# Optimization experiments

Measured on AMD Instinct MI355X. Metric: run time of the kernel, lower is better.

The kernel has to match this reference:

```python
import jax, jax.numpy as jnp
import numpy as np

EPS = 1e-5

def _ln(x):
    m = jnp.mean(x, axis=-1, keepdims=True)
    v = jnp.mean((x - m) ** 2, axis=-1, keepdims=True)
    return (x - m) / jnp.sqrt(v + EPS)

def setup_inputs() -> dict:
    key = jax.random.key(0)
    ks = jax.random.split(key, 6)
    B, S, E, H = 2, 2048, 1024, 16
    sd = 1.0 / np.sqrt(E)
    x = jax.random.normal(ks[0], (B, S, E), dtype=jnp.float32)
    w_in = jax.random.normal(ks[1], (3 * E, E), dtype=jnp.float32) * sd
    w_out = jax.random.normal(ks[2], (E, E), dtype=jnp.float32) * sd
    w_fc = jax.random.normal(ks[3], (4 * E, E), dtype=jnp.float32) * sd
    b_fc = jnp.zeros((4 * E,), dtype=jnp.float32)
    w_proj = jax.random.normal(ks[4], (E, 4 * E), dtype=jnp.float32) * (1.0 / np.sqrt(4 * E))
    b_proj = jnp.zeros((E,), dtype=jnp.float32)
    return {"x": x, "w_in": w_in, "w_out": w_out, "w_fc": w_fc,
            "b_fc": b_fc, "w_proj": w_proj, "b_proj": b_proj}

def reference(x, w_in, w_out, w_fc, b_fc, w_proj, b_proj):
    B, S, E = x.shape
    H = 16
    D = E // H
    h = _ln(x)
    qkv = h @ w_in.T                      # [B,S,3E]
    q, k, v = jnp.split(qkv, 3, axis=-1)
    q = q.reshape(B, S, H, D)
    k = k.reshape(B, S, H, D)
    v = v.reshape(B, S, H, D)
    scale = 1.0 / np.sqrt(D)
    scores = jnp.einsum('bqhd,bkhd->bhqk', q, k) * scale  # [B,H,S,S]
    causal = jnp.tril(jnp.ones((S, S), dtype=bool))
    scores = jnp.where(causal, scores, -jnp.inf)
    attn = jax.nn.softmax(scores, axis=-1)
    o = jnp.einsum('bhqk,bkhd->bqhd', attn, v).reshape(B, S, E)
    attn_out = o @ w_out.T
    x2 = x + attn_out                      # residual 1
    h2 = _ln(x2)
    m = jax.nn.relu(h2 @ w_fc.T + b_fc)    # [B,S,4E]
    return (m @ w_proj.T + b_proj) + x2    # residual 2
```

## Files before the change

### kernel.cpp

```cpp
#include <hip/hip_runtime.h>
#include <stdint.h>

#define AS1 __attribute__((address_space(1)))
#define AS3 __attribute__((address_space(3)))

typedef __bf16 bf8_t __attribute__((ext_vector_type(8)));
typedef float f4_t __attribute__((ext_vector_type(4)));
typedef unsigned short ush;

__device__ __forceinline__ ush f2b(float f) {
  unsigned u = __builtin_bit_cast(unsigned, f);
  u += 0x7fffu + ((u >> 16) & 1u);
  return (ush)(u >> 16);
}
__device__ __forceinline__ void unpack8(uint4 u, float* dst) {
  unsigned a0 = u.x, a1 = u.y, a2 = u.z, a3 = u.w;
  dst[0] = __builtin_bit_cast(float, a0 << 16);
  dst[1] = __builtin_bit_cast(float, a0 & 0xffff0000u);
  dst[2] = __builtin_bit_cast(float, a1 << 16);
  dst[3] = __builtin_bit_cast(float, a1 & 0xffff0000u);
  dst[4] = __builtin_bit_cast(float, a2 << 16);
  dst[5] = __builtin_bit_cast(float, a2 & 0xffff0000u);
  dst[6] = __builtin_bit_cast(float, a3 << 16);
  dst[7] = __builtin_bit_cast(float, a3 & 0xffff0000u);
}

__global__ __launch_bounds__(256) void f2b_all(
    const float* __restrict__ w_in, const float* __restrict__ w_out,
    const float* __restrict__ w_fc, const float* __restrict__ w_proj,
    ush* __restrict__ o_in, ush* __restrict__ o_out,
    ush* __restrict__ o_fc, ush* __restrict__ o_proj) {
  const int blk = blockIdx.x;
  const float* src;
  ush* dst;
  int base;
  if (blk < 3072) { src = w_in; dst = o_in; base = blk; }
  else if (blk < 4096) { src = w_out; dst = o_out; base = blk - 3072; }
  else if (blk < 8192) { src = w_fc; dst = o_fc; base = blk - 4096; }
  else { src = w_proj; dst = o_proj; base = blk - 8192; }
  const int i = (base * 256 + threadIdx.x) * 4;
  float4 v = *(const float4*)(src + i);
  union { ush u[4]; uint2 d; } p;
  p.u[0] = f2b(v.x); p.u[1] = f2b(v.y); p.u[2] = f2b(v.z); p.u[3] = f2b(v.w);
  *(uint2*)(dst + i) = p.d;
}

__global__ __launch_bounds__(256) void ln_kernel(const float* __restrict__ x,
                                                 ush* __restrict__ out) {
  const int row = blockIdx.x, tid = threadIdx.x;
  const float* xr = x + (size_t)row * 1024;
  float4 v = ((const float4*)xr)[tid];
  float s = v.x + v.y + v.z + v.w;
  float q = v.x * v.x + v.y * v.y + v.z * v.z + v.w * v.w;
  for (int o = 32; o; o >>= 1) { s += __shfl_down(s, o); q += __shfl_down(q, o); }
  __shared__ float rs[4], rq[4];
  const int w = tid >> 6;
  if ((tid & 63) == 0) { rs[w] = s; rq[w] = q; }
  __syncthreads();
  s = rs[0] + rs[1] + rs[2] + rs[3];
  q = rq[0] + rq[1] + rq[2] + rq[3];
  const float mean = s * (1.0f / 1024.0f);
  const float var = q * (1.0f / 1024.0f) - mean * mean;
  const float rstd = rsqrtf(var + 1e-5f);
  union { ush u[4]; uint2 d; } p;
  p.u[0] = f2b((v.x - mean) * rstd);
  p.u[1] = f2b((v.y - mean) * rstd);
  p.u[2] = f2b((v.z - mean) * rstd);
  p.u[3] = f2b((v.w - mean) * rstd);
  *(uint2*)(out + (size_t)row * 1024 + tid * 4) = p.d;
}

template <int EPI, int BM, int MINW>
__global__ __launch_bounds__(256, MINW) void gemm_bt(
    const ush* __restrict__ A, const ush* __restrict__ Bw,
    int M, int N, int K,
    const float* __restrict__ bias, const float* __restrict__ resid,
    float* __restrict__ outF, ush* __restrict__ outB) {
  constexpr int MI = BM / 32;
  constexpr int NCH = (BM + 128) / 16;
  constexpr int PC = NCH / 4;
  constexpr int ASZ = BM * 32;
  __shared__ ush lds[2 * ASZ + 2 * 4096];
  const int tid = threadIdx.x;
  const int wave = tid >> 6, lane = tid & 63;
  const int bm = blockIdx.x, bn = blockIdx.y;
  const int wm = (wave & 1) * (BM / 2), wn = (wave >> 1) * 64;
  const int l16 = lane & 15, quad = lane >> 4;
  const int srow = lane >> 2;
  const int scol = (lane & 3) * 8;

  const ush* Abase = A + (size_t)(bm * BM) * K;
  const ush* Bbase = Bw + (size_t)(bn * 128) * K;

  f4_t acc[MI][4];
#pragma unroll
  for (int i = 0; i < MI; ++i)
#pragma unroll
    for (int j = 0; j < 4; ++j) acc[i][j] = (f4_t){0.f, 0.f, 0.f, 0.f};

  const int kiters = K >> 5;

  auto stage = [&](int k0, int buf) {
    const int kk = k0 * 32;
#pragma unroll
    for (int i = 0; i < PC; ++i) {
      const int c = wave * PC + i;
      if (c < BM / 16) {
        const ush* ga = Abase + (size_t)(c * 16 + srow) * K + kk + scol;
        __builtin_amdgcn_global_load_lds((const AS1 void*)ga,
                                         (AS3 void*)(lds + buf * ASZ + c * 512), 16, 0, 0);
      } else {
        const int c2 = c - BM / 16;
        const ush* gb = Bbase + (size_t)(c2 * 16 + srow) * K + kk + scol;
        __builtin_amdgcn_global_load_lds(
            (const AS1 void*)gb, (AS3 void*)(lds + 2 * ASZ + buf * 4096 + c2 * 512), 16, 0, 0);
      }
    }
  };

  stage(0, 0);
  __syncthreads();
  for (int k0 = 0; k0 < kiters; ++k0) {
    const int cur = k0 & 1;
    if (k0 + 1 < kiters) stage(k0 + 1, cur ^ 1);
    bf8_t af[MI], bfr[4];
#pragma unroll
    for (int mi = 0; mi < MI; ++mi)
      af[mi] = *(const bf8_t*)&lds[cur * ASZ + (wm + mi * 16 + l16) * 32 + quad * 8];
#pragma unroll
    for (int ni = 0; ni < 4; ++ni)
      bfr[ni] = *(const bf8_t*)&lds[2 * ASZ + cur * 4096 + (wn + ni * 16 + l16) * 32 + quad * 8];
#pragma unroll
    for (int mi = 0; mi < MI; ++mi)
#pragma unroll
      for (int ni = 0; ni < 4; ++ni)
        acc[mi][ni] =
            __builtin_amdgcn_mfma_f32_16x16x32_bf16(af[mi], bfr[ni], acc[mi][ni], 0, 0, 0);
    __syncthreads();
  }

  if (EPI == 0 || EPI == 2) {
    ush* eb = lds + wave * ASZ;
#pragma unroll
    for (int mi = 0; mi < MI; ++mi)
#pragma unroll
      for (int ni = 0; ni < 4; ++ni) {
        const int gn = bn * 128 + wn + ni * 16 + l16;
        const float bv = (EPI == 2) ? bias[gn] : 0.0f;
#pragma unroll
        for (int r = 0; r < 4; ++r) {
          float v = acc[mi][ni][r] + bv;
          if (EPI == 2) v = fmaxf(v, 0.0f);
          eb[(mi * 16 + quad * 4 + r) * 64 + ni * 16 + l16] = f2b(v);
        }
      }
#pragma unroll
    for (int j = 0; j < BM / 16; ++j) {
      const int lr = j * 8 + (lane >> 3);
      const int c8 = (lane & 7) * 8;
      uint4 v = *(const uint4*)&eb[lr * 64 + c8];
      *(uint4*)(outB + (size_t)(bm * BM + wm + lr) * N + bn * 128 + wn + c8) = v;
    }
  } else {
#pragma unroll
    for (int mi = 0; mi < MI; ++mi) {
#pragma unroll
      for (int ni = 0; ni < 4; ++ni) {
        const int gm0 = bm * BM + wm + mi * 16 + quad * 4;
        const int gn = bn * 128 + wn + ni * 16 + l16;
        const float bv = (EPI == 3) ? bias[gn] : 0.0f;
#pragma unroll
        for (int r = 0; r < 4; ++r) {
          const size_t idx = (size_t)(gm0 + r) * N + gn;
          outF[idx] = acc[mi][ni][r] + bv + resid[idx];
        }
      }
    }
  }
}

__global__ __launch_bounds__(256) void pack_kv(const ush* __restrict__ qkv,
                                               ush* __restrict__ Kp,
                                               ush* __restrict__ Vp) {
  const int lin = blockIdx.x;
  const int kt = lin & 31, h = (lin >> 5) & 15, b = lin >> 9;
  const int tid = threadIdx.x;
  __shared__ ush Vs[64 * 72];
  const size_t rowbase = (size_t)(b * 2048 + kt * 64) * 3072 + h * 64;
  ush* Kt = Kp + (size_t)lin * 4096;
  ush* Vt = Vp + (size_t)lin * 4096;

  const int r0 = tid >> 3, cin = tid & 7;
#pragma unroll
  for (int it = 0; it < 2; ++it) {
    const int r = r0 + it * 32;
    uint4 ku = *(const uint4*)(qkv + rowbase + (size_t)r * 3072 + 1024 + cin * 8);
    float f[8]; unpack8(ku, f);
    union { ush us[8]; uint4 v; } pk;
#pragma unroll
    for (int j = 0; j < 8; ++j) pk.us[j] = f2b(f[j] * 0.125f);
    *(uint4*)(Kt + (size_t)(r * 8 + (cin ^ (r & 7))) * 8) = pk.v;
    uint4 vu = *(const uint4*)(qkv + rowbase + (size_t)r * 3072 + 2048 + cin * 8);
    *(uint4*)&Vs[r * 72 + cin * 8] = vu;
  }
  __syncthreads();
#pragma unroll
  for (int oc2 = 0; oc2 < 2; ++oc2) {
    const int oc = tid * 2 + oc2;
    const int d = oc >> 3, c = oc & 7;
    const int k0 = 8 * (c ^ (d & 7));
    union { ush us[8]; uint4 v; } pk;
#pragma unroll
    for (int j = 0; j < 8; ++j) pk.us[j] = Vs[(k0 + j) * 72 + d];
    *(uint4*)(Vt + (size_t)oc * 8) = pk.v;
  }
}

__global__ __launch_bounds__(256, 4) void attn_kernel(const ush* __restrict__ qkv,
                                                      const ush* __restrict__ Kp,
                                                      const ush* __restrict__ Vp,
                                                      ush* __restrict__ o) {
  const int lin = blockIdx.x;
  const int b = lin & 1, h = (lin >> 1) & 15, tq = lin >> 5;
  const int tid = threadIdx.x;
  const int wave = tid >> 6, lane = tid & 63;
  const int l15 = lane & 15, quad = lane >> 4;

  __shared__ __align__(16) ush Ks[64 * 64];
  __shared__ __align__(16) ush Vt[64 * 64];
  __shared__ __align__(16) ush Ps[64 * 72];

  bf8_t qf[2];
  {
    const int qrow = b * 2048 + tq * 64 + wave * 16 + l15;
#pragma unroll
    for (int s = 0; s < 2; ++s) {
      union { uint4 u; bf8_t v; } pk;
      pk.u = *(const uint4*)(qkv + (size_t)qrow * 3072 + h * 64 + s * 32 + quad * 8);
      qf[s] = pk.v;
    }
  }

  float m_s = -1e30f, l_s = 0.f;
  f4_t O[4];
#pragma unroll
  for (int j = 0; j < 4; ++j) O[j] = (f4_t){0.f, 0.f, 0.f, 0.f};

  const int qw0 = tq * 64 + wave * 16;
  const int swz = (l15 & 7) * 8;
  const size_t tile0 = (size_t)((b * 16 + h) * 32) * 4096;

  for (int kt = 0; kt <= tq; ++kt) {
    __syncthreads();
    const ush* Ktile = Kp + tile0 + (size_t)kt * 4096;
    const ush* Vtile = Vp + tile0 + (size_t)kt * 4096;
#pragma unroll
    for (int i = 0; i < 2; ++i) {
      const int seg = wave * 2 + i;
      __builtin_amdgcn_global_load_lds((const AS1 void*)(Ktile + seg * 512 + lane * 8),
                                       (AS3 void*)(Ks + seg * 512), 16, 0, 0);
      __builtin_amdgcn_global_load_lds((const AS1 void*)(Vtile + seg * 512 + lane * 8),
                                       (AS3 void*)(Vt + seg * 512), 16, 0, 0);
    }
    __syncthreads();

    f4_t S[4];
#pragma unroll
    for (int mi = 0; mi < 4; ++mi) S[mi] = (f4_t){0.f, 0.f, 0.f, 0.f};
#pragma unroll
    for (int s = 0; s < 2; ++s)
#pragma unroll
      for (int mi = 0; mi < 4; ++mi) {
        bf8_t kf = *(const bf8_t*)&Ks[(mi * 16 + l15) * 64 + (((4 * s + quad) * 8) ^ swz)];
        S[mi] = __builtin_amdgcn_mfma_f32_16x16x32_bf16(kf, qf[s], S[mi], 0, 0, 0);
      }

    if (kt == tq) {
#pragma unroll
      for (int mi = 0; mi < 4; ++mi)
#pragma unroll
        for (int r = 0; r < 4; ++r) {
          const int kg = kt * 64 + mi * 16 + quad * 4 + r;
          const int qg = qw0 + l15;
          if (kg > qg) S[mi][r] = -1e30f;
        }
    }

    float mx = -1e30f;
#pragma unroll
    for (int mi = 0; mi < 4; ++mi)
#pragma unroll
      for (int r = 0; r < 4; ++r) mx = fmaxf(mx, S[mi][r]);
    mx = fmaxf(mx, __shfl_xor(mx, 16));
    mx = fmaxf(mx, __shfl_xor(mx, 32));
    const float mn = fmaxf(m_s, mx);
    const float alpha = __expf(m_s - mn);
    float sum = 0.f;
#pragma unroll
    for (int mi = 0; mi < 4; ++mi)
#pragma unroll
      for (int r = 0; r < 4; ++r) {
        const float p = __expf(S[mi][r] - mn);
        S[mi][r] = p;
        sum += p;
      }
    sum += __shfl_xor(sum, 16);
    sum += __shfl_xor(sum, 32);
    m_s = mn;
    l_s = l_s * alpha + sum;
#pragma unroll
    for (int mi = 0; mi < 4; ++mi) {
      uint2 w2;
      w2.x = (unsigned)f2b(S[mi][0]) | ((unsigned)f2b(S[mi][1]) << 16);
      w2.y = (unsigned)f2b(S[mi][2]) | ((unsigned)f2b(S[mi][3]) << 16);
      *(uint2*)&Ps[(wave * 16 + l15) * 72 + mi * 16 + quad * 4] = w2;
    }

    bf8_t pf[2], vf[4][2];
#pragma unroll
    for (int s = 0; s < 2; ++s)
      pf[s] = *(const bf8_t*)&Ps[(wave * 16 + l15) * 72 + s * 32 + quad * 8];
#pragma unroll
    for (int n4 = 0; n4 < 4; ++n4)
#pragma unroll
      for (int s = 0; s < 2; ++s)
        vf[n4][s] = *(const bf8_t*)&Vt[(n4 * 16 + l15) * 64 + (((4 * s + quad) * 8) ^ swz)];
    float ar[4];
#pragma unroll
    for (int r = 0; r < 4; ++r) ar[r] = __shfl(alpha, quad * 4 + r);
#pragma unroll
    for (int n4 = 0; n4 < 4; ++n4) {
#pragma unroll
      for (int r = 0; r < 4; ++r) O[n4][r] *= ar[r];
#pragma unroll
      for (int s = 0; s < 2; ++s)
        O[n4] = __builtin_amdgcn_mfma_f32_16x16x32_bf16(pf[s], vf[n4][s], O[n4], 0, 0, 0);
    }
  }

  const float rc = 1.0f / l_s;
  float rr[4];
#pragma unroll
  for (int r = 0; r < 4; ++r) rr[r] = __shfl(rc, quad * 4 + r);
#pragma unroll
  for (int n4 = 0; n4 < 4; ++n4)
#pragma unroll
    for (int r = 0; r < 4; ++r) {
      const int qg = tq * 64 + wave * 16 + quad * 4 + r;
      o[(size_t)(b * 2048 + qg) * 1024 + h * 64 + n4 * 16 + l15] = f2b(O[n4][r] * rr[r]);
    }
}

extern "C" void kernel_launch(void* const* d_in, const int* in_sizes, int n_in,
                              void* d_out, int out_size, void* d_ws, size_t ws_size,
                              hipStream_t stream) {
  const float* x = (const float*)d_in[0];
  const float* w_in = (const float*)d_in[1];
  const float* w_out = (const float*)d_in[2];
  const float* w_fc = (const float*)d_in[3];
  const float* b_fc = (const float*)d_in[4];
  const float* w_proj = (const float*)d_in[5];
  const float* b_proj = (const float*)d_in[6];
  float* out = (float*)d_out;

  char* ws = (char*)d_ws;
  ush* w_in_b = (ush*)(ws);
  ush* w_out_b = (ush*)(ws + 6291456);
  ush* w_fc_b = (ush*)(ws + 8388608);
  ush* w_proj_b = (ush*)(ws + 16777216);
  ush* h_b = (ush*)(ws + 25165824);
  float* x2 = (float*)(ws + 33554432);
  ush* qkv_b = (ush*)(ws + 50331648);
  ush* o_b = (ush*)(ws + 75497472);
  ush* m_b = (ush*)(ws + 50331648);
  ush* Kp = (ush*)(ws + 83886080);
  ush* Vp = (ush*)(ws + 92274688);

  f2b_all<<<12288, 256, 0, stream>>>(w_in, w_out, w_fc, w_proj,
                                     w_in_b, w_out_b, w_fc_b, w_proj_b);

  ln_kernel<<<4096, 256, 0, stream>>>(x, h_b);

  gemm_bt<0, 128, 2><<<dim3(32, 24), 256, 0, stream>>>(
      h_b, w_in_b, 4096, 3072, 1024, nullptr, nullptr, nullptr, qkv_b);

  pack_kv<<<1024, 256, 0, stream>>>(qkv_b, Kp, Vp);

  attn_kernel<<<1024, 256, 0, stream>>>(qkv_b, Kp, Vp, o_b);

  gemm_bt<1, 64, 4><<<dim3(64, 8), 256, 0, stream>>>(
      o_b, w_out_b, 4096, 1024, 1024, nullptr, x, x2, nullptr);

  ln_kernel<<<4096, 256, 0, stream>>>(x2, h_b);

  gemm_bt<2, 128, 2><<<dim3(32, 32), 256, 0, stream>>>(
      h_b, w_fc_b, 4096, 4096, 1024, b_fc, nullptr, nullptr, m_b);

  gemm_bt<3, 64, 4><<<dim3(64, 8), 256, 0, stream>>>(
      m_b, w_proj_b, 4096, 1024, 4096, b_proj, x2, out, nullptr);
}
```

Baseline: 338.1 us.

## Load GEMM fragments directly from global into registers, dropping LDS staging

The GEMM kernel no longer stages A and B tiles through shared memory with async global-to-LDS loads. Each wave now reads its MFMA operand fragments straight from global memory into registers, prefetching the next k-step, and the per-iteration barriers are gone. The two large GEMMs also move from 128-row to 64-row tiles with more blocks. This removes LDS traffic and synchronisation, but each wave fetches its own data, so reuse across waves in a block is lost. That raises global/L2 traffic, and each lane's 16-byte reads are strided by K, so coalescing is poor.

```diff
diff --git a/kernel.cpp b/kernel.cpp
--- a/kernel.cpp
+++ b/kernel.cpp
@@ -70,27 +70,23 @@
   *(uint2*)(out + (size_t)row * 1024 + tid * 4) = p.d;
 }
 
-template <int EPI, int BM, int MINW>
-__global__ __launch_bounds__(256, MINW) void gemm_bt(
+template <int EPI, int MINW>
+__global__ __launch_bounds__(256, MINW) void gemm_rr(
     const ush* __restrict__ A, const ush* __restrict__ Bw,
     int M, int N, int K,
     const float* __restrict__ bias, const float* __restrict__ resid,
     float* __restrict__ outF, ush* __restrict__ outB) {
-  constexpr int MI = BM / 32;
-  constexpr int NCH = (BM + 128) / 16;
-  constexpr int PC = NCH / 4;
-  constexpr int ASZ = BM * 32;
-  __shared__ ush lds[2 * ASZ + 2 * 4096];
+  constexpr int BM = 64;
+  constexpr int MI = 2;
+  __shared__ ush eb[4 * 32 * 64];
   const int tid = threadIdx.x;
   const int wave = tid >> 6, lane = tid & 63;
   const int bm = blockIdx.x, bn = blockIdx.y;
-  const int wm = (wave & 1) * (BM / 2), wn = (wave >> 1) * 64;
+  const int wm = (wave & 1) * 32, wn = (wave >> 1) * 64;
   const int l16 = lane & 15, quad = lane >> 4;
-  const int srow = lane >> 2;
-  const int scol = (lane & 3) * 8;
-
-  const ush* Abase = A + (size_t)(bm * BM) * K;
-  const ush* Bbase = Bw + (size_t)(bn * 128) * K;
+
+  const ush* Ab = A + (size_t)(bm * BM + wm + l16) * K + quad * 8;
+  const ush* Bb = Bw + (size_t)(bn * 128 + wn + l16) * K + quad * 8;
 
   f4_t acc[MI][4];
 #pragma unroll
@@ -100,47 +96,37 @@
 
   const int kiters = K >> 5;
 
-  auto stage = [&](int k0, int buf) {
-    const int kk = k0 * 32;
-#pragma unroll
-    for (int i = 0; i < PC; ++i) {
-      const int c = wave * PC + i;
-      if (c < BM / 16) {
-        const ush* ga = Abase + (size_t)(c * 16 + srow) * K + kk + scol;
-        __builtin_amdgcn_global_load_lds((const AS1 void*)ga,
-                                         (AS3 void*)(lds + buf * ASZ + c * 512), 16, 0, 0);
-      } else {
-        const int c2 = c - BM / 16;
-        const ush* gb = Bbase + (size_t)(c2 * 16 + srow) * K + kk + scol;
-        __builtin_amdgcn_global_load_lds(
-            (const AS1 void*)gb, (AS3 void*)(lds + 2 * ASZ + buf * 4096 + c2 * 512), 16, 0, 0);
-      }
-    }
-  };
-
-  stage(0, 0);
-  __syncthreads();
+  uint4 apf[MI], bpf[4];
+#pragma unroll
+  for (int mi = 0; mi < MI; ++mi) apf[mi] = *(const uint4*)(Ab + (size_t)mi * 16 * K);
+#pragma unroll
+  for (int ni = 0; ni < 4; ++ni) bpf[ni] = *(const uint4*)(Bb + (size_t)ni * 16 * K);
+
   for (int k0 = 0; k0 < kiters; ++k0) {
-    const int cur = k0 & 1;
-    if (k0 + 1 < kiters) stage(k0 + 1, cur ^ 1);
     bf8_t af[MI], bfr[4];
 #pragma unroll
-    for (int mi = 0; mi < MI; ++mi)
-      af[mi] = *(const bf8_t*)&lds[cur * ASZ + (wm + mi * 16 + l16) * 32 + quad * 8];
-#pragma unroll
-    for (int ni = 0; ni < 4; ++ni)
-      bfr[ni] = *(const bf8_t*)&lds[2 * ASZ + cur * 4096 + (wn + ni * 16 + l16) * 32 + quad * 8];
+    for (int mi = 0; mi < MI; ++mi) af[mi] = __builtin_bit_cast(bf8_t, apf[mi]);
+#pragma unroll
+    for (int ni = 0; ni < 4; ++ni) bfr[ni] = __builtin_bit_cast(bf8_t, bpf[ni]);
+    if (k0 + 1 < kiters) {
+      const int kk = (k0 + 1) * 32;
+#pragma unroll
+      for (int mi = 0; mi < MI; ++mi)
+        apf[mi] = *(const uint4*)(Ab + (size_t)mi * 16 * K + kk);
+#pragma unroll
+      for (int ni = 0; ni < 4; ++ni)
+        bpf[ni] = *(const uint4*)(Bb + (size_t)ni * 16 * K + kk);
+    }
 #pragma unroll
     for (int mi = 0; mi < MI; ++mi)
 #pragma unroll
       for (int ni = 0; ni < 4; ++ni)
         acc[mi][ni] =
             __builtin_amdgcn_mfma_f32_16x16x32_bf16(af[mi], bfr[ni], acc[mi][ni], 0, 0, 0);
-    __syncthreads();
   }
 
   if (EPI == 0 || EPI == 2) {
-    ush* eb = lds + wave * ASZ;
+    ush* ebw = eb + wave * 32 * 64;
 #pragma unroll
     for (int mi = 0; mi < MI; ++mi)
 #pragma unroll
@@ -151,14 +137,14 @@
         for (int r = 0; r < 4; ++r) {
           float v = acc[mi][ni][r] + bv;
           if (EPI == 2) v = fmaxf(v, 0.0f);
-          eb[(mi * 16 + quad * 4 + r) * 64 + ni * 16 + l16] = f2b(v);
+          ebw[(mi * 16 + quad * 4 + r) * 64 + ni * 16 + l16] = f2b(v);
         }
       }
 #pragma unroll
-    for (int j = 0; j < BM / 16; ++j) {
+    for (int j = 0; j < 4; ++j) {
       const int lr = j * 8 + (lane >> 3);
       const int c8 = (lane & 7) * 8;
-      uint4 v = *(const uint4*)&eb[lr * 64 + c8];
+      uint4 v = *(const uint4*)&ebw[lr * 64 + c8];
       *(uint4*)(outB + (size_t)(bm * BM + wm + lr) * N + bn * 128 + wn + c8) = v;
     }
   } else {
@@ -381,21 +367,21 @@
 
   ln_kernel<<<4096, 256, 0, stream>>>(x, h_b);
 
-  gemm_bt<0, 128, 2><<<dim3(32, 24), 256, 0, stream>>>(
+  gemm_rr<0, 4><<<dim3(64, 24), 256, 0, stream>>>(
       h_b, w_in_b, 4096, 3072, 1024, nullptr, nullptr, nullptr, qkv_b);
 
   pack_kv<<<1024, 256, 0, stream>>>(qkv_b, Kp, Vp);
 
   attn_kernel<<<1024, 256, 0, stream>>>(qkv_b, Kp, Vp, o_b);
 
-  gemm_bt<1, 64, 4><<<dim3(64, 8), 256, 0, stream>>>(
+  gemm_rr<1, 4><<<dim3(64, 8), 256, 0, stream>>>(
       o_b, w_out_b, 4096, 1024, 1024, nullptr, x, x2, nullptr);
 
   ln_kernel<<<4096, 256, 0, stream>>>(x2, h_b);
 
-  gemm_bt<2, 128, 2><<<dim3(32, 32), 256, 0, stream>>>(
+  gemm_rr<2, 4><<<dim3(64, 32), 256, 0, stream>>>(
       h_b, w_fc_b, 4096, 4096, 1024, b_fc, nullptr, nullptr, m_b);
 
-  gemm_bt<3, 64, 4><<<dim3(64, 8), 256, 0, stream>>>(
+  gemm_rr<3, 4><<<dim3(64, 8), 256, 0, stream>>>(
       m_b, w_proj_b, 4096, 1024, 4096, b_proj, x2, out, nullptr);
 }
```

Measured after the change: 697.9 us. 106% more time.
